# Performance work log

Measured on AMD Instinct MI355X. Metric: run time of the kernel, lower is better.

## Reference

```python
import jax, jax.numpy as jnp
import numpy as np

K = 2            # kernel_size per dim
DIM = 3          # pseudo-coordinate dim
NUM_COMBOS = K ** DIM  # 8 spline weight matrices
BITS = np.array([[(b >> d) & 1 for d in range(DIM)] for b in range(NUM_COMBOS)], dtype=np.int32)  # [8,3]
STRIDE = np.array([1, K, K * K], dtype=np.int32)  # weight-index strides per dim
GRID_DIV = 4
POOL_SIZE = 25.0  # 100 / 4
NUM_GRIDS = GRID_DIV * GRID_DIV
EPS = 1e-5


def spline_conv(x, src, dst, pseudo, W, n_nodes):
    """torch_spline_conv, degree=1, open splines, root_weight=False, aggr='mean'."""
    v = pseudo * (K - 1)          # [E,3] in [0, K-1]
    lo = jnp.floor(v)
    frac = v - lo                 # [E,3]
    lo = lo.astype(jnp.int32)
    x_src = x[src]                # [E, in]
    msg = jnp.zeros((x_src.shape[0], W.shape[2]), x.dtype)
    for b in range(NUM_COMBOS):
        bits = BITS[b]            # [3]
        # basis weight: prod over dims of (frac if bit else 1-frac)
        w_b = jnp.prod(jnp.where(bits == 1, frac, 1.0 - frac), axis=1)  # [E]
        idx = jnp.sum(jnp.clip(lo + bits, 0, K - 1) * STRIDE, axis=1)   # [E] in [0,7]
        Wb = W[idx]               # [E, in, out] (irregular gather)
        msg = msg + w_b[:, None] * jnp.einsum('ei,eio->eo', x_src, Wb)
    s = jax.ops.segment_sum(msg, dst, num_segments=n_nodes)
    cnt = jax.ops.segment_sum(jnp.ones((msg.shape[0], 1), msg.dtype), dst, num_segments=n_nodes)
    return s / jnp.maximum(cnt, 1.0)  # mean aggregation


def batch_norm(x, gamma, beta):
    mu = jnp.mean(x, axis=0)
    var = jnp.mean((x - mu) ** 2, axis=0)  # biased, as torch BN training normalization
    return (x - mu) * jax.lax.rsqrt(var + EPS) * gamma + beta


def max_pool_grid(x, pos2):
    cell = jnp.clip(jnp.floor(pos2 / POOL_SIZE).astype(jnp.int32), 0, GRID_DIV - 1)  # [N,2]
    cluster = cell[:, 0] + GRID_DIV * cell[:, 1]                                      # [N]
    pooled = jax.ops.segment_max(x, cluster, num_segments=NUM_GRIDS)                  # [16,C]
    return jnp.where(jnp.isfinite(pooled), pooled, 0.0)  # empty cells -> 0


def setup_inputs() -> dict:
    key = jax.random.key(0)
    ks = jax.random.split(key, 8)
    N, E = 262144, 4194304
    x = jax.random.normal(ks[0], (N, 1), jnp.float32)
    edge_index = jax.random.randint(ks[1], (2, E), 0, N, dtype=jnp.int64)
    edge_attr = jax.random.uniform(ks[2], (E, 3), jnp.float32)          # pseudo coords in [0,1]
    pos = jax.random.uniform(ks[3], (N, 2), jnp.float32) * 100.0        # spatial coords in [0,100)
    W1 = jax.random.normal(ks[4], (8, 1, 2), jnp.float32)
    W2 = jax.random.normal(ks[5], (8, 2, 4), jnp.float32)
    fc_w = jax.random.normal(ks[6], (4, 64), jnp.float32) * 0.1
    return {"x": x, "edge_index": edge_index, "edge_attr": edge_attr, "pos": pos,
            "W1": W1, "W2": W2,
            "gamma1": jnp.ones((2,), jnp.float32), "beta1": jnp.zeros((2,), jnp.float32),
            "gamma2": jnp.ones((4,), jnp.float32), "beta2": jnp.zeros((4,), jnp.float32),
            "fc_w": fc_w}


def reference(x, edge_index, edge_attr, pos, W1, W2, gamma1, beta1, gamma2, beta2, fc_w):
    n = x.shape[0]
    src, dst = edge_index[0], edge_index[1]
    h = spline_conv(x, src, dst, edge_attr, W1, n)   # [N,2]
    h = jax.nn.elu(h)
    h = batch_norm(h, gamma1, beta1)
    h = spline_conv(h, src, dst, edge_attr, W2, n)   # [N,4]
    h = batch_norm(h, gamma2, beta2)
    pooled = max_pool_grid(h, pos)                   # [16,4]
    flat = pooled.reshape(1, NUM_GRIDS * 4)          # [1,64]
    return flat @ fc_w.T                             # [1,4]
```

## Files before the change

### kernel.cpp

```cpp
#include <hip/hip_runtime.h>


#define TPB 256
#define NODES_PER_BUCK 512
#define BUCK_SHIFT 9
#define NBUCK 512
#define BPART 512
#define REGN 40
#define SCAP1 5120

typedef unsigned long long u64;
typedef unsigned int u32;

__device__ __forceinline__ void basis_weights(float f0, float f1, float f2, float w[8]) {
    float g0 = 1.f - f0, g1 = 1.f - f1, g2 = 1.f - f2;
    w[0] = g0 * g1 * g2;  w[1] = f0 * g1 * g2;
    w[2] = g0 * f1 * g2;  w[3] = f0 * f1 * g2;
    w[4] = g0 * g1 * f2;  w[5] = f0 * g1 * f2;
    w[6] = g0 * f1 * f2;  w[7] = f0 * f1 * f2;
}

__device__ __forceinline__ u64 pack_rec(int src, int dloc, float f0, float f1, float f2) {
    u32 q0 = (u32)(f0 * 4095.f + 0.5f);
    u32 q1 = (u32)(f1 * 4095.f + 0.5f);
    u32 q2 = (u32)(f2 * 4095.f + 0.5f);
    return (u64)(u32)src | ((u64)(u32)dloc << 18)
         | ((u64)q0 << 27) | ((u64)q1 << 39) | ((u64)q2 << 51);
}

__global__ void hist_kernel(const int* __restrict__ ei, int E,
                            u32* __restrict__ cntArr ) {
    __shared__ u32 h[NBUCK];
    for (int i = threadIdx.x; i < NBUCK; i += TPB) h[i] = 0u;
    __syncthreads();
    int ch = (E + BPART - 1) / BPART;
    int s = blockIdx.x * ch;
    int e_end = min(E, s + ch);
    int e = s + threadIdx.x * 4;
    for (; e + 4 <= e_end; e += TPB * 4) {
        int4 d4 = *(const int4*)&ei[E + e];
        atomicAdd(&h[d4.x >> BUCK_SHIFT], 1u);
        atomicAdd(&h[d4.y >> BUCK_SHIFT], 1u);
        atomicAdd(&h[d4.z >> BUCK_SHIFT], 1u);
        atomicAdd(&h[d4.w >> BUCK_SHIFT], 1u);
    }
    for (e = e_end - (e_end - s) % (TPB * 4) + threadIdx.x; e < e_end; e += TPB)
        atomicAdd(&h[ei[E + e] >> BUCK_SHIFT], 1u);
    __syncthreads();
    for (int i = threadIdx.x; i < NBUCK; i += TPB)
        cntArr[i * BPART + blockIdx.x] = h[i];
}

__global__ void scan512_kernel(u32* __restrict__ data,
                               u32* __restrict__ totals) {
    __shared__ u32 s[BPART];
    int t = threadIdx.x, g = blockIdx.x;
    u32 v = data[g * BPART + t];
    s[t] = v;
    __syncthreads();
    for (int o = 1; o < BPART; o <<= 1) {
        u32 u = (t >= o) ? s[t - o] : 0u;
        __syncthreads();
        s[t] += u;
        __syncthreads();
    }
    data[g * BPART + t] = s[t] - v;
    if (t == BPART - 1) totals[g] = s[t];
}

__global__ void scanbase_kernel(const u32* __restrict__ in,
                                u32* __restrict__ excl) {
    __shared__ u32 s[NBUCK];
    int t = threadIdx.x;
    u32 v = in[t];
    s[t] = v;
    __syncthreads();
    for (int o = 1; o < NBUCK; o <<= 1) {
        u32 u = (t >= o) ? s[t - o] : 0u;
        __syncthreads();
        s[t] += u;
        __syncthreads();
    }
    excl[t] = s[t] - v;
}

__global__ void scatter_kernel(const int* __restrict__ ei,
                               const float* __restrict__ attr,
                               const u32* __restrict__ bktBase,
                               const u32* __restrict__ preArr,
                               u64* __restrict__ part1, int E) {
    __shared__ u32 cursor[NBUCK];
    for (int i = threadIdx.x; i < NBUCK; i += TPB)
        cursor[i] = bktBase[i] + preArr[i * BPART + blockIdx.x];
    __syncthreads();
    int ch = (E + BPART - 1) / BPART;
    int s = blockIdx.x * ch;
    int e_end = min(E, s + ch);
    int e = s + threadIdx.x * 4;
    for (; e + 4 <= e_end; e += TPB * 4) {
        int4 s4 = *(const int4*)&ei[e];
        int4 d4 = *(const int4*)&ei[E + e];
        float4 a0 = *(const float4*)&attr[3 * e];
        float4 a1 = *(const float4*)&attr[3 * e + 4];
        float4 a2 = *(const float4*)&attr[3 * e + 8];
        int srcs[4] = {s4.x, s4.y, s4.z, s4.w};
        int dsts[4] = {d4.x, d4.y, d4.z, d4.w};
        float f[4][3] = {{a0.x, a0.y, a0.z}, {a0.w, a1.x, a1.y},
                         {a1.z, a1.w, a2.x}, {a2.y, a2.z, a2.w}};
#pragma unroll
        for (int j = 0; j < 4; j++) {
            u32 pos = atomicAdd(&cursor[dsts[j] >> BUCK_SHIFT], 1u);
            part1[pos] = pack_rec(srcs[j], dsts[j] & (NODES_PER_BUCK - 1),
                                  f[j][0], f[j][1], f[j][2]);
        }
    }
    for (e = e_end - (e_end - s) % (TPB * 4) + threadIdx.x; e < e_end; e += TPB) {
        int src = ei[e], dst = ei[E + e];
        u32 pos = atomicAdd(&cursor[dst >> BUCK_SHIFT], 1u);
        part1[pos] = pack_rec(src, dst & (NODES_PER_BUCK - 1),
                              attr[3 * e], attr[3 * e + 1], attr[3 * e + 2]);
    }
}

__global__ void __launch_bounds__(TPB)
fused_agg1_kernel(const u64* __restrict__ part1,
                  const u32* __restrict__ bktBase,
                  const u32* __restrict__ bktTot,
                  const float* __restrict__ x,
                  const float* __restrict__ W1,
                  u32* __restrict__ deg,
                  u32* __restrict__ off,
                  float* __restrict__ h1,
                  float* __restrict__ accum ) {
    __shared__ u64 stage[SCAP1];
    __shared__ u32 hist[NODES_PER_BUCK];
    __shared__ u32 obase[NODES_PER_BUCK];
    __shared__ u32 ss[TPB];
    __shared__ u32 midsh;
    __shared__ float rbuf[4][4];
    int t = threadIdx.x, g = blockIdx.x;
    u32 s = bktBase[g], n_e = bktTot[g];
    hist[t] = 0u; hist[t + TPB] = 0u;
    u64 rec[REGN];
#pragma unroll
    for (int k = 0; k < REGN; k++) {
        u32 i = (u32)t + (u32)k * TPB;
        rec[k] = (i < n_e) ? part1[s + i] : 0ull;
    }
    __syncthreads();
#pragma unroll
    for (int k = 0; k < REGN; k++) {
        u32 i = (u32)t + (u32)k * TPB;
        if (i < n_e)
            atomicAdd(&hist[(u32)(rec[k] >> 18) & (NODES_PER_BUCK - 1)], 1u);
    }
    for (u32 i = (u32)t + REGN * TPB; i < n_e; i += TPB)
        atomicAdd(&hist[(u32)(part1[s + i] >> 18) & (NODES_PER_BUCK - 1)], 1u);
    __syncthreads();
    u32 c0 = hist[2 * t], c1 = hist[2 * t + 1];
    u32 tsum = c0 + c1;
    ss[t] = tsum;
    __syncthreads();
    for (int o = 1; o < TPB; o <<= 1) {
        u32 u = (t >= o) ? ss[t - o] : 0u;
        __syncthreads();
        ss[t] += u;
        __syncthreads();
    }
    u32 ex = ss[t] - tsum;
    obase[2 * t] = ex;
    obase[2 * t + 1] = ex + c0;
    int n0 = (g << BUCK_SHIFT) + 2 * t;
    deg[n0] = c0; deg[n0 + 1] = c1;
    off[n0] = s + ex; off[n0 + 1] = s + ex + c0;
    hist[2 * t] = ex;
    hist[2 * t + 1] = ex + c0;
    if (t == 127) midsh = ss[127];
    __syncthreads();
    u32 mid = midsh;
    float ts0 = 0.f, ts1 = 0.f, tq0 = 0.f, tq1 = 0.f;
    for (int h = 0; h < 2; h++) {
        u32 pstart = h ? mid : 0u;
        u32 plen = h ? (n_e - mid) : mid;
        if (plen > (u32)SCAP1) plen = (u32)SCAP1;
#pragma unroll
        for (int k = 0; k < REGN; k++) {
            u32 i = (u32)t + (u32)k * TPB;
            if (i < n_e) {
                u32 loc = (u32)(rec[k] >> 18) & (NODES_PER_BUCK - 1);
                if ((int)(loc >> 8) == h) {
                    u32 pos = atomicAdd(&hist[loc], 1u);
                    u32 li = pos - pstart;
                    if (li < (u32)SCAP1) stage[li] = rec[k];
                }
            }
        }
        for (u32 i = (u32)t + REGN * TPB; i < n_e; i += TPB) {
            u64 r = part1[s + i];
            u32 loc = (u32)(r >> 18) & (NODES_PER_BUCK - 1);
            if ((int)(loc >> 8) == h) {
                u32 pos = atomicAdd(&hist[loc], 1u);
                u32 li = pos - pstart;
                if (li < (u32)SCAP1) stage[li] = r;
            }
        }
        __syncthreads();
        int ln = h * 256 + t;
        u32 st = obase[ln] - pstart;
        u32 en = hist[ln] - pstart;
        u32 d = hist[ln] - obase[ln];
        if (en > plen) en = plen;
        if (st > plen) st = plen;
        float s0 = 0.f, s1 = 0.f;
        for (u32 j = st; j < en; ++j) {
            u64 r = stage[j];
            float xv = x[(u32)r & 0x3FFFFu];
            float f0 = (float)((u32)(r >> 27) & 0xFFFu) * (1.f / 4095.f);
            float f1 = (float)((u32)(r >> 39) & 0xFFFu) * (1.f / 4095.f);
            float f2 = (float)((u32)(r >> 51) & 0xFFFu) * (1.f / 4095.f);
            float w[8];
            basis_weights(f0, f1, f2, w);
            float wv0 = 0.f, wv1 = 0.f;
#pragma unroll
            for (int b = 0; b < 8; b++) {
                wv0 += w[b] * W1[2 * b];
                wv1 += w[b] * W1[2 * b + 1];
            }
            s0 += xv * wv0;
            s1 += xv * wv1;
        }
        float cm = d > 1u ? (float)d : 1.f;
        float a = s0 / cm, b = s1 / cm;
        a = a > 0.f ? a : (__expf(a) - 1.f);
        b = b > 0.f ? b : (__expf(b) - 1.f);
        int n = (g << BUCK_SHIFT) + ln;
        *(float2*)&h1[2 * n] = make_float2(a, b);
        ts0 += a; tq0 += a * a;
        ts1 += b; tq1 += b * b;
        __syncthreads();
    }
#pragma unroll
    for (int o = 32; o > 0; o >>= 1) {
        ts0 += __shfl_down(ts0, o, 64);
        ts1 += __shfl_down(ts1, o, 64);
        tq0 += __shfl_down(tq0, o, 64);
        tq1 += __shfl_down(tq1, o, 64);
    }
    int wv = t >> 6;
    if ((t & 63) == 0) {
        rbuf[wv][0] = ts0; rbuf[wv][1] = ts1;
        rbuf[wv][2] = tq0; rbuf[wv][3] = tq1;
    }
    __syncthreads();
    if (t < 4) {
        float v = rbuf[0][t] + rbuf[1][t] + rbuf[2][t] + rbuf[3][t];
        atomicAdd(&accum[t], v);
    }
}

__global__ void bnparams_kernel(const float* __restrict__ accum,
                                const float* __restrict__ gamma,
                                const float* __restrict__ beta,
                                float* __restrict__ params, int C, float invN) {
    int c = threadIdx.x;
    if (c < C) {
        float mu  = accum[c] * invN;
        float var = accum[C + c] * invN - mu * mu;
        float sc  = gamma[c] * rsqrtf(var + 1e-5f);
        params[c] = sc;
        params[C + c] = beta[c] - mu * sc;
    }
}

__global__ void __launch_bounds__(TPB)
agg2_kernel(const u64* __restrict__ part1,
            const u32* __restrict__ bktBase,
            const u32* __restrict__ bktTot,
            const u32* __restrict__ off,
            const u32* __restrict__ deg,
            const float* __restrict__ h1,
            const float* __restrict__ W2,
            const float* __restrict__ params,
            float* __restrict__ h2,
            float* __restrict__ accum ) {
    __shared__ u64 stage[SCAP1];
    __shared__ u32 hist[NODES_PER_BUCK];
    __shared__ u32 obase[NODES_PER_BUCK];
    __shared__ u32 segend[NODES_PER_BUCK];
    __shared__ float rbuf[4][8];
    int t = threadIdx.x, g = blockIdx.x;
    u32 s = bktBase[g], n_e = bktTot[g];
    int nb = (g << BUCK_SHIFT);
#pragma unroll
    for (int k = 0; k < 2; k++) {
        int i = t + k * TPB;
        u32 o = off[nb + i] - s;
        u32 dd = deg[nb + i];
        obase[i] = o;
        segend[i] = o + dd;
        hist[i] = o;
    }
    u64 rec[REGN];
#pragma unroll
    for (int k = 0; k < REGN; k++) {
        u32 i = (u32)t + (u32)k * TPB;
        rec[k] = (i < n_e) ? part1[s + i] : 0ull;
    }
    float sc0 = params[0], sc1 = params[1], sh0 = params[2], sh1 = params[3];
    __syncthreads();
    u32 mid = obase[256];
    float ts[4] = {0.f, 0.f, 0.f, 0.f}, tq[4] = {0.f, 0.f, 0.f, 0.f};
    for (int h = 0; h < 2; h++) {
        u32 pstart = h ? mid : 0u;
        u32 plen = h ? (n_e - mid) : mid;
        if (plen > (u32)SCAP1) plen = (u32)SCAP1;
#pragma unroll
        for (int k = 0; k < REGN; k++) {
            u32 i = (u32)t + (u32)k * TPB;
            if (i < n_e) {
                u32 loc = (u32)(rec[k] >> 18) & (NODES_PER_BUCK - 1);
                if ((int)(loc >> 8) == h) {
                    u32 pos = atomicAdd(&hist[loc], 1u);
                    u32 li = pos - pstart;
                    if (li < (u32)SCAP1) stage[li] = rec[k];
                }
            }
        }
        for (u32 i = (u32)t + REGN * TPB; i < n_e; i += TPB) {
            u64 r = part1[s + i];
            u32 loc = (u32)(r >> 18) & (NODES_PER_BUCK - 1);
            if ((int)(loc >> 8) == h) {
                u32 pos = atomicAdd(&hist[loc], 1u);
                u32 li = pos - pstart;
                if (li < (u32)SCAP1) stage[li] = r;
            }
        }
        __syncthreads();
        int ln = h * 256 + t;
        u32 st = obase[ln] - pstart;
        u32 en = segend[ln] - pstart;
        u32 d = segend[ln] - obase[ln];
        if (en > plen) en = plen;
        if (st > plen) st = plen;
        float m0 = 0.f, m1 = 0.f, m2 = 0.f, m3 = 0.f;
        for (u32 j = st; j < en; ++j) {
            u64 r = stage[j];
            float2 hv = *(const float2*)&h1[2 * ((u32)r & 0x3FFFFu)];
            float a = hv.x * sc0 + sh0;
            float b = hv.y * sc1 + sh1;
            float f0 = (float)((u32)(r >> 27) & 0xFFFu) * (1.f / 4095.f);
            float f1 = (float)((u32)(r >> 39) & 0xFFFu) * (1.f / 4095.f);
            float f2 = (float)((u32)(r >> 51) & 0xFFFu) * (1.f / 4095.f);
            float w[8];
            basis_weights(f0, f1, f2, w);
#pragma unroll
            for (int bb = 0; bb < 8; bb++) {
                float wa = w[bb] * a, wb = w[bb] * b;
                m0 += wa * W2[8 * bb + 0] + wb * W2[8 * bb + 4];
                m1 += wa * W2[8 * bb + 1] + wb * W2[8 * bb + 5];
                m2 += wa * W2[8 * bb + 2] + wb * W2[8 * bb + 6];
                m3 += wa * W2[8 * bb + 3] + wb * W2[8 * bb + 7];
            }
        }
        float cm = d > 1u ? (float)d : 1.f;
        m0 /= cm; m1 /= cm; m2 /= cm; m3 /= cm;
        int n = nb + ln;
        float4 o4; o4.x = m0; o4.y = m1; o4.z = m2; o4.w = m3;
        *(float4*)&h2[4 * n] = o4;
        ts[0] += m0; tq[0] += m0 * m0;
        ts[1] += m1; tq[1] += m1 * m1;
        ts[2] += m2; tq[2] += m2 * m2;
        ts[3] += m3; tq[3] += m3 * m3;
        __syncthreads();
    }
#pragma unroll
    for (int o = 32; o > 0; o >>= 1) {
#pragma unroll
        for (int ch = 0; ch < 4; ch++) {
            ts[ch] += __shfl_down(ts[ch], o, 64);
            tq[ch] += __shfl_down(tq[ch], o, 64);
        }
    }
    int wv = t >> 6;
    if ((t & 63) == 0) {
#pragma unroll
        for (int ch = 0; ch < 4; ch++) {
            rbuf[wv][ch] = ts[ch];
            rbuf[wv][4 + ch] = tq[ch];
        }
    }
    __syncthreads();
    if (t < 8) {
        float v = rbuf[0][t] + rbuf[1][t] + rbuf[2][t] + rbuf[3][t];
        atomicAdd(&accum[t], v);
    }
}

__device__ __forceinline__ unsigned enc_float(float v) {
    unsigned u = __float_as_uint(v);
    return (v >= 0.f) ? (u | 0x80000000u) : ~u;
}

__global__ void pool_kernel(const float* __restrict__ h2,
                            const float* __restrict__ pos,
                            const float* __restrict__ params,
                            unsigned* __restrict__ pooled, int N) {
    __shared__ unsigned lmax[64];
    for (int i = threadIdx.x; i < 64; i += blockDim.x) lmax[i] = 0u;
    __syncthreads();
    float sc[4], sh[4];
#pragma unroll
    for (int c = 0; c < 4; c++) { sc[c] = params[c]; sh[c] = params[4 + c]; }
    int stride = gridDim.x * blockDim.x;
    for (int n = blockIdx.x * blockDim.x + threadIdx.x; n < N; n += stride) {
        float px = pos[2 * n + 0], py = pos[2 * n + 1];
        int cx = (int)floorf(px * (1.f / 25.f));
        int cy = (int)floorf(py * (1.f / 25.f));
        cx = min(max(cx, 0), 3);
        cy = min(max(cy, 0), 3);
        int cl = cx + 4 * cy;
        float4 h = *(const float4*)&h2[4 * n];
        atomicMax(&lmax[4 * cl + 0], enc_float(h.x * sc[0] + sh[0]));
        atomicMax(&lmax[4 * cl + 1], enc_float(h.y * sc[1] + sh[1]));
        atomicMax(&lmax[4 * cl + 2], enc_float(h.z * sc[2] + sh[2]));
        atomicMax(&lmax[4 * cl + 3], enc_float(h.w * sc[3] + sh[3]));
    }
    __syncthreads();
    for (int i = threadIdx.x; i < 64; i += blockDim.x)
        if (lmax[i]) atomicMax(&pooled[i], lmax[i]);
}

__global__ void final_kernel(const unsigned* __restrict__ pooled,
                             const float* __restrict__ fcw,
                             float* __restrict__ out) {
    __shared__ float p[64];
    int t = threadIdx.x;
    if (t < 64) {
        unsigned u = pooled[t];
        float v = 0.f;
        if (u != 0u) {
            unsigned bits = (u & 0x80000000u) ? (u ^ 0x80000000u) : ~u;
            v = __uint_as_float(bits);
        }
        p[t] = v;
    }
    __syncthreads();
    if (t < 4) {
        float s = 0.f;
        for (int k = 0; k < 64; k++) s += p[k] * fcw[t * 64 + k];
        out[t] = s;
    }
}

extern "C" void kernel_launch(void* const* d_in, const int* in_sizes, int n_in,
                              void* d_out, int out_size, void* d_ws, size_t ws_size,
                              hipStream_t stream) {
    const float* x      = (const float*)d_in[0];
    const int*   ei     = (const int*)d_in[1];
    const float* attr   = (const float*)d_in[2];
    const float* pos    = (const float*)d_in[3];
    const float* W1     = (const float*)d_in[4];
    const float* W2     = (const float*)d_in[5];
    const float* gamma1 = (const float*)d_in[6];
    const float* beta1  = (const float*)d_in[7];
    const float* gamma2 = (const float*)d_in[8];
    const float* beta2  = (const float*)d_in[9];
    const float* fcw    = (const float*)d_in[10];
    float* out = (float*)d_out;

    const int N = in_sizes[0];
    const int E = in_sizes[2] / 3;

    u64* part1 = (u64*)d_ws;
    float* base = (float*)(part1 + E);
    float* accum  = base;
    float* params = base + 12;
    unsigned* pooled = (unsigned*)(base + 24);
    u32* cntArr  = (u32*)(base + 88);
    u32* bktTot  = cntArr + (size_t)NBUCK * BPART;
    u32* bktBase = bktTot + NBUCK;
    u32* deg     = bktBase + NBUCK;
    u32* off     = deg + N;
    float* h1 = (float*)(off + N);
    float* h2 = h1 + 2 * (size_t)N;

    hipMemsetAsync(base, 0, 88 * sizeof(float), stream);

    hist_kernel<<<BPART, TPB, 0, stream>>>(ei, E, cntArr);
    scan512_kernel<<<NBUCK, BPART, 0, stream>>>(cntArr, bktTot);
    scanbase_kernel<<<1, NBUCK, 0, stream>>>(bktTot, bktBase);
    scatter_kernel<<<BPART, TPB, 0, stream>>>(ei, attr, bktBase, cntArr, part1, E);
    fused_agg1_kernel<<<NBUCK, TPB, 0, stream>>>(part1, bktBase, bktTot, x, W1,
                                                 deg, off, h1, accum);
    bnparams_kernel<<<1, 64, 0, stream>>>(accum, gamma1, beta1, params, 2,
                                          1.0f / (float)N);
    agg2_kernel<<<NBUCK, TPB, 0, stream>>>(part1, bktBase, bktTot, off, deg,
                                           h1, W2, params, h2, accum + 4);
    bnparams_kernel<<<1, 64, 0, stream>>>(accum + 4, gamma2, beta2, params + 4, 4,
                                          1.0f / (float)N);
    pool_kernel<<<512, 256, 0, stream>>>(h2, pos, params + 4, pooled, N);
    final_kernel<<<1, 64, 0, stream>>>(pooled, fcw, out);
}
```

Baseline: 290.8 us.

## Stage scatter records in LDS sorted by bucket before global write

The scatter kernel now processes edges in 4096-edge chunks. Each chunk gets a local bucket histogram, a block-wide scan and an LDS staging pass, so records for the same bucket are written to global memory in contiguous runs instead of random per-edge positions. The aim is to improve write coalescing for part1. In exchange it adds several barriers per chunk, a 256-step scan, large LDS use (about 42KB) that lowers occupancy, and non-vectorized input loads.

```diff
diff --git a/kernel.cpp b/kernel.cpp
--- a/kernel.cpp
+++ b/kernel.cpp
@@ -8,9 +8,12 @@
 #define BPART 512
 #define REGN 40
 #define SCAP1 5120
+#define CHUNK 4096
+#define EPT 16
 
 typedef unsigned long long u64;
 typedef unsigned int u32;
+typedef unsigned short u16;
 
 __device__ __forceinline__ void basis_weights(float f0, float f1, float f2, float w[8]) {
     float g0 = 1.f - f0, g1 = 1.f - f1, g2 = 1.f - f2;
@@ -84,41 +87,73 @@
     excl[t] = s[t] - v;
 }
 
-__global__ void scatter_kernel(const int* __restrict__ ei,
-                               const float* __restrict__ attr,
-                               const u32* __restrict__ bktBase,
-                               const u32* __restrict__ preArr,
-                               u64* __restrict__ part1, int E) {
-    __shared__ u32 cursor[NBUCK];
-    for (int i = threadIdx.x; i < NBUCK; i += TPB)
-        cursor[i] = bktBase[i] + preArr[i * BPART + blockIdx.x];
-    __syncthreads();
+__global__ void __launch_bounds__(TPB)
+scatter_kernel(const int* __restrict__ ei,
+               const float* __restrict__ attr,
+               const u32* __restrict__ bktBase,
+               const u32* __restrict__ preArr,
+               u64* __restrict__ part1, int E) {
+    __shared__ u64 stage[CHUNK];
+    __shared__ u16 bid[CHUNK];
+    __shared__ u32 cnt[NBUCK];
+    __shared__ u32 cbase[NBUCK];
+    __shared__ u32 gcur[NBUCK];
+    __shared__ u32 ss[TPB];
+    int t = threadIdx.x, blk = blockIdx.x;
+    for (int i = t; i < NBUCK; i += TPB)
+        gcur[i] = bktBase[i] + preArr[i * BPART + blk];
     int ch = (E + BPART - 1) / BPART;
-    int s = blockIdx.x * ch;
-    int e_end = min(E, s + ch);
-    int e = s + threadIdx.x * 4;
-    for (; e + 4 <= e_end; e += TPB * 4) {
-        int4 s4 = *(const int4*)&ei[e];
-        int4 d4 = *(const int4*)&ei[E + e];
-        float4 a0 = *(const float4*)&attr[3 * e];
-        float4 a1 = *(const float4*)&attr[3 * e + 4];
-        float4 a2 = *(const float4*)&attr[3 * e + 8];
-        int srcs[4] = {s4.x, s4.y, s4.z, s4.w};
-        int dsts[4] = {d4.x, d4.y, d4.z, d4.w};
-        float f[4][3] = {{a0.x, a0.y, a0.z}, {a0.w, a1.x, a1.y},
-                         {a1.z, a1.w, a2.x}, {a2.y, a2.z, a2.w}};
-#pragma unroll
-        for (int j = 0; j < 4; j++) {
-            u32 pos = atomicAdd(&cursor[dsts[j] >> BUCK_SHIFT], 1u);
-            part1[pos] = pack_rec(srcs[j], dsts[j] & (NODES_PER_BUCK - 1),
-                                  f[j][0], f[j][1], f[j][2]);
-        }
-    }
-    for (e = e_end - (e_end - s) % (TPB * 4) + threadIdx.x; e < e_end; e += TPB) {
-        int src = ei[e], dst = ei[E + e];
-        u32 pos = atomicAdd(&cursor[dst >> BUCK_SHIFT], 1u);
-        part1[pos] = pack_rec(src, dst & (NODES_PER_BUCK - 1),
-                              attr[3 * e], attr[3 * e + 1], attr[3 * e + 2]);
+    int s0 = blk * ch;
+    int e_end = min(E, s0 + ch);
+    for (int cs = s0; cs < e_end; cs += CHUNK) {
+        int cn = min(CHUNK, e_end - cs);
+        cnt[t] = 0u; cnt[t + TPB] = 0u;
+        __syncthreads();
+        u64 rec[EPT]; u32 bb[EPT], rk[EPT];
+#pragma unroll
+        for (int k = 0; k < EPT; k++) {
+            int e = cs + t + k * TPB;
+            if (e < e_end) {
+                int src = ei[e], dst = ei[E + e];
+                rec[k] = pack_rec(src, dst & (NODES_PER_BUCK - 1),
+                                  attr[3 * e], attr[3 * e + 1], attr[3 * e + 2]);
+                bb[k] = (u32)dst >> BUCK_SHIFT;
+                rk[k] = atomicAdd(&cnt[bb[k]], 1u);
+            }
+        }
+        __syncthreads();
+        u32 c0 = cnt[2 * t], c1 = cnt[2 * t + 1];
+        u32 tsum = c0 + c1;
+        ss[t] = tsum;
+        __syncthreads();
+        for (int o = 1; o < TPB; o <<= 1) {
+            u32 u = (t >= o) ? ss[t - o] : 0u;
+            __syncthreads();
+            ss[t] += u;
+            __syncthreads();
+        }
+        u32 ex = ss[t] - tsum;
+        cbase[2 * t] = ex;
+        cbase[2 * t + 1] = ex + c0;
+        __syncthreads();
+#pragma unroll
+        for (int k = 0; k < EPT; k++) {
+            int e = cs + t + k * TPB;
+            if (e < e_end) {
+                u32 p = cbase[bb[k]] + rk[k];
+                stage[p] = rec[k];
+                bid[p] = (u16)bb[k];
+            }
+        }
+        __syncthreads();
+        for (int i = t; i < cn; i += TPB) {
+            u32 b = (u32)bid[i];
+            part1[gcur[b] + ((u32)i - cbase[b])] = stage[i];
+        }
+        __syncthreads();
+        gcur[2 * t] += c0;
+        gcur[2 * t + 1] += c1;
+        __syncthreads();
     }
 }
 
```

After: 262.0 us. -9.9%, faster.
